# Kernel tuning notes

Measured on AMD Instinct MI355X. Metric: run time of the kernel, lower is better.

## Reference

```python
import jax, jax.numpy as jnp
import numpy as np

NUM_HEADS = 8
EPS = 1e-6


def conv1x1(x, w, b):
    # x: [b,c,h,w], w: [out,in], b: [out]  (torch Conv2d 1x1 weight squeezed)
    return jnp.einsum('bchw,oc->bohw', x, w) + b[None, :, None, None]


def feature_map(x):
    return jax.nn.elu(x) + 1.0


def setup_inputs() -> dict:
    key = jax.random.key(0)
    ks = jax.random.split(key, 9)
    C = 512
    s = 1.0 / np.sqrt(C)
    x = jax.random.normal(ks[0], (8, C, 64, 64), dtype=jnp.float32)
    wq = jax.random.normal(ks[1], (C, C), dtype=jnp.float32) * s
    wk = jax.random.normal(ks[2], (C, C), dtype=jnp.float32) * s
    wv = jax.random.normal(ks[3], (C, C), dtype=jnp.float32) * s
    wo = jax.random.normal(ks[4], (C, C), dtype=jnp.float32) * s
    bq = jax.random.normal(ks[5], (C,), dtype=jnp.float32) * 0.01
    bk = jax.random.normal(ks[6], (C,), dtype=jnp.float32) * 0.01
    bv = jax.random.normal(ks[7], (C,), dtype=jnp.float32) * 0.01
    bo = jax.random.normal(ks[8], (C,), dtype=jnp.float32) * 0.01
    return {'x': x, 'wq': wq, 'bq': bq, 'wk': wk, 'bk': bk,
            'wv': wv, 'bv': bv, 'wo': wo, 'bo': bo}


def reference(x, wq, bq, wk, bk, wv, bv, wo, bo):
    b, c, h, w = x.shape
    nh = NUM_HEADS
    hd = c // nh
    L = h * w

    def to_heads(t):
        # [b,c,h,w] -> [b,nh,L,hd]
        return t.reshape(b, nh, hd, L).transpose(0, 1, 3, 2)

    Q = feature_map(to_heads(conv1x1(x, wq, bq)))
    K = feature_map(to_heads(conv1x1(x, wk, bk)))
    V = to_heads(conv1x1(x, wv, bv)) / L  # values / v_length

    KV = jnp.einsum('bhld,bhlv->bhdv', K, V)                 # [b,nh,hd,hd]
    Z = 1.0 / (jnp.einsum('bhld,bhd->bhl', Q, K.sum(axis=-2)) + EPS)
    out = jnp.einsum('bhld,bhdv,bhl->bhlv', Q, KV, Z) * L    # [b,nh,L,hd]

    out = out.transpose(0, 1, 3, 2).reshape(b, c, h, w)
    return conv1x1(out, wo, bo)
```

## Files before the change

### kernel.cpp

```cpp
#include <hip/hip_runtime.h>
#include <hip/hip_bf16.h>
#include <stdint.h>

#define BATCH 8
#define CCH   512
#define NHD   8
#define HD    64
#define LLEN  4096
#define M1    1536

typedef __bf16 bf16x8 __attribute__((ext_vector_type(8)));
typedef __bf16 bf16x4 __attribute__((ext_vector_type(4)));
typedef float  f32x4  __attribute__((ext_vector_type(4)));

__device__ __forceinline__ f32x4 mfma16(bf16x8 a, bf16x8 b, f32x4 c) {
  return __builtin_amdgcn_mfma_f32_16x16x32_bf16(a, b, c, 0, 0, 0);
}

__device__ __forceinline__ void gload_lds16(const void* g, void* l) {
  __builtin_amdgcn_global_load_lds(
      (const __attribute__((address_space(1))) uint32_t*)(uintptr_t)g,
      (__attribute__((address_space(3))) uint32_t*)(uintptr_t)l,
      16, 0, 0);
}

__global__ void pack_w(const float* __restrict__ wq, const float* __restrict__ wk,
                       const float* __restrict__ wv, const float* __restrict__ wo,
                       const float* __restrict__ bq, const float* __restrict__ bk,
                       const float* __restrict__ bv,
                       __bf16* __restrict__ wqkvb, __bf16* __restrict__ wob,
                       float* __restrict__ biasq) {
  const int n = M1 * CCH + CCH * CCH + M1;
  for (int i = blockIdx.x * blockDim.x + threadIdx.x; i < n; i += gridDim.x * blockDim.x) {
    if (i < M1 * CCH) {
      int r = i >> 9, c = i & 511;
      float v = (r < 512) ? wq[r * 512 + c]
              : (r < 1024) ? wk[(r - 512) * 512 + c]
                           : wv[(r - 1024) * 512 + c];
      wqkvb[i] = (__bf16)v;
    } else if (i < M1 * CCH + CCH * CCH) {
      int j = i - M1 * CCH;
      wob[j] = (__bf16)wo[j];
    } else {
      int j = i - M1 * CCH - CCH * CCH;
      biasq[j] = (j < 512) ? bq[j] : (j < 1024) ? bk[j - 512] : bv[j - 1024];
    }
  }
}

__global__ __launch_bounds__(256) void transpose_x(const float* __restrict__ x,
                                                   __bf16* __restrict__ xt) {
  __shared__ float tile[64][65];
  const int b = blockIdx.z, c0 = blockIdx.y * 64, l0 = blockIdx.x * 64;
  const int t = threadIdx.x;
  const int lq = (t & 15) * 4, cr = t >> 4;
  const float* xp = x + ((size_t)b * CCH + c0) * LLEN + l0;
#pragma unroll
  for (int q = 0; q < 4; ++q) {
    const int c = cr + q * 16;
    float4 v = *(const float4*)(xp + (size_t)c * LLEN + lq);
    tile[c][lq + 0] = v.x;
    tile[c][lq + 1] = v.y;
    tile[c][lq + 2] = v.z;
    tile[c][lq + 3] = v.w;
  }
  __syncthreads();
  __bf16* xo = xt + ((size_t)b * LLEN + l0) * CCH + c0;
  const int c8 = (t & 7) * 8, lr = t >> 3;
#pragma unroll
  for (int p = 0; p < 2; ++p) {
    const int l = lr + p * 32;
    bf16x8 o;
#pragma unroll
    for (int i = 0; i < 8; ++i) o[i] = (__bf16)tile[c8 + i][l];
    *(bf16x8*)(xo + (size_t)l * CCH + c8) = o;
  }
}

#define STG128(tt, buf)                                                      \
  {                                                                          \
    const __bf16* As_ = Ag + (tt) * 32;                                      \
    const __bf16* Bs_ = Bg + (tt) * 32;                                      \
    __bf16* dA = lds + (buf) * 8192;                                         \
    __bf16* dB = dA + 4096;                                                  \
    gload_lds16(As_ + srcOff1, dA + tid * 8);                                \
    gload_lds16(As_ + srcOff2, dA + tid * 8 + 2048);                         \
    gload_lds16(Bs_ + srcOff1, dB + tid * 8);                                \
    gload_lds16(Bs_ + srcOff2, dB + tid * 8 + 2048);                         \
  }

template <int EPI>
__global__ __launch_bounds__(256, 4) void gemm128(
    const __bf16* __restrict__ A, const __bf16* __restrict__ Bm,
    const float* __restrict__ bias,
    __bf16* __restrict__ qt, __bf16* __restrict__ kcm, __bf16* __restrict__ vcm,
    float* __restrict__ out) {
  __shared__ __attribute__((aligned(16))) __bf16 lds[17408];
  const int b  = blockIdx.z;
  const int n0 = blockIdx.x * 128;
  const int m0 = blockIdx.y * 128;
  const int tid = threadIdx.x;
  const int ll = tid & 63, w = tid >> 6;
  const int wr = w >> 1, wc = w & 1;
  const int lhi = ll >> 4, llo = ll & 15;

  const int slotE = ((lhi ^ ((llo >> 1) & 3)) << 3);
  int aOff[4], bOff[4];
#pragma unroll
  for (int m = 0; m < 4; ++m) aOff[m] = (wr * 64 + m * 16 + llo) * 32 + slotE;
#pragma unroll
  for (int n = 0; n < 4; ++n) bOff[n] = 4096 + (wc * 64 + n * 16 + llo) * 32 + slotE;

  const int s1 = tid, s2 = tid + 256;
  const int r1 = s1 >> 2, r2s = s2 >> 2;
  const int srcOff1 = r1 * CCH + (((s1 & 3) ^ ((r1 >> 1) & 3)) << 3);
  const int srcOff2 = r2s * CCH + (((s2 & 3) ^ ((r2s >> 1) & 3)) << 3);

  const __bf16* Ag = A + (size_t)m0 * CCH;
  const __bf16* Bg = Bm + ((size_t)b * LLEN + n0) * CCH;

  f32x4 acc[4][4] = {};

  STG128(0, 0)
  __syncthreads();

  for (int t = 0; t < 16; ++t) {
    const int buf = t & 1;
    if (t < 15) STG128(t + 1, buf ^ 1)
    bf16x8 af[4], bfr[4];
    const __bf16* base = lds + buf * 8192;
#pragma unroll
    for (int m = 0; m < 4; ++m) af[m] = *(const bf16x8*)(base + aOff[m]);
#pragma unroll
    for (int n = 0; n < 4; ++n) bfr[n] = *(const bf16x8*)(base + bOff[n]);
#pragma unroll
    for (int m = 0; m < 4; ++m)
#pragma unroll
      for (int n = 0; n < 4; ++n) acc[m][n] = mfma16(af[m], bfr[n], acc[m][n]);
    __syncthreads();
  }

  if (EPI == 0) {
    if (m0 < 512) {
#pragma unroll
      for (int i = 0; i < 4; ++i)
#pragma unroll
        for (int j = 0; j < 4; ++j) {
          const int chq = wr * 64 + i * 16 + lhi * 4;
          const int lq  = wc * 64 + j * 16 + llo;
          bf16x4 pk;
#pragma unroll
          for (int r = 0; r < 4; ++r) {
            float tv = acc[i][j][r] + bias[m0 + chq + r];
            tv = tv > 0.f ? tv + 1.f : __expf(tv);
            pk[r] = (__bf16)tv;
          }
          *(bf16x4*)(lds + lq * 136 + chq) = pk;
        }
      __syncthreads();
      const int l = tid >> 1, seg = tid & 1;
      __bf16* dst = qt + ((size_t)b * LLEN + n0 + l) * CCH + m0 + seg * 64;
      const __bf16* src = lds + l * 136 + seg * 64;
#pragma unroll
      for (int k = 0; k < 8; ++k)
        *(bf16x8*)(dst + k * 8) = *(const bf16x8*)(src + k * 8);
    } else {
      const bool isK = (m0 < 1024);
      __bf16* base_out = isK ? kcm + ((size_t)b * CCH + (m0 - 512)) * LLEN
                             : vcm + ((size_t)b * CCH + (m0 - 1024)) * LLEN;
#pragma unroll
      for (int i = 0; i < 4; ++i)
#pragma unroll
        for (int j = 0; j < 4; ++j) {
          const int chq = wr * 64 + i * 16 + lhi * 4;
          const int lq  = wc * 64 + j * 16 + llo;
#pragma unroll
          for (int r = 0; r < 4; ++r) {
            float tv = acc[i][j][r] + bias[m0 + chq + r];
            if (isK) tv = tv > 0.f ? tv + 1.f : __expf(tv);
            lds[(chq + r) * 136 + lq] = (__bf16)tv;
          }
        }
      __syncthreads();
      const int ch = tid >> 1, seg = tid & 1;
      __bf16* dst = base_out + (size_t)ch * LLEN + n0 + seg * 64;
      const __bf16* src = lds + ch * 136 + seg * 64;
#pragma unroll
      for (int k = 0; k < 8; ++k)
        *(bf16x8*)(dst + k * 8) = *(const bf16x8*)(src + k * 8);
    }
  } else {
    float* flds = (float*)lds;
#pragma unroll
    for (int p = 0; p < 2; ++p) {
      if (p) __syncthreads();
#pragma unroll
      for (int i = 0; i < 4; ++i)
#pragma unroll
        for (int jj = 0; jj < 2; ++jj) {
          const int j = p * 2 + jj;
          const int chq = wr * 64 + i * 16 + lhi * 4;
          const int cc  = wc * 32 + jj * 16 + llo;
#pragma unroll
          for (int r = 0; r < 4; ++r)
            flds[(chq + r) * 68 + cc] = acc[i][j][r] + bias[m0 + chq + r];
        }
      __syncthreads();
      const int ch = tid >> 1, half = tid & 1;
      float* dst = out + ((size_t)b * CCH + m0 + ch) * LLEN + n0 + half * 64 + p * 32;
      const float* src = flds + ch * 68 + half * 32;
#pragma unroll
      for (int k = 0; k < 8; ++k)
        *(float4*)(dst + k * 4) = *(const float4*)(src + k * 4);
    }
  }
}

__global__ __launch_bounds__(256) void kv_part_k(const __bf16* __restrict__ kcm,
                                                 const __bf16* __restrict__ vcm,
                                                 float* __restrict__ part,
                                                 float* __restrict__ part_ks) {
  __shared__ float red[8192];
  __shared__ float ksred[4][64];
  const int lc = blockIdx.x, bh = blockIdx.y;
  const int b = bh >> 3, h = bh & 7;
  const int tid = threadIdx.x;
  const int w = tid >> 6, ll = tid & 63, lhi = ll >> 4, llo = ll & 15;
  const __bf16* Kp = kcm + ((size_t)b * CCH + h * 64) * LLEN;
  const __bf16* Vp = vcm + ((size_t)b * CCH + h * 64) * LLEN;
  f32x4 acc[4][4];
#pragma unroll
  for (int i = 0; i < 4; ++i)
#pragma unroll
    for (int j = 0; j < 4; ++j) acc[i][j] = (f32x4){0.f, 0.f, 0.f, 0.f};
  float ks[4] = {0.f, 0.f, 0.f, 0.f};
  const int base = lc * 512 + w * 128 + lhi * 8;
#pragma unroll
  for (int kt = 0; kt < 4; ++kt) {
    const int k0 = base + kt * 32;
    bf16x8 af[4], bfr[4];
#pragma unroll
    for (int i = 0; i < 4; ++i) af[i]  = *(const bf16x8*)(Kp + (size_t)(i * 16 + llo) * LLEN + k0);
#pragma unroll
    for (int i = 0; i < 4; ++i) bfr[i] = *(const bf16x8*)(Vp + (size_t)(i * 16 + llo) * LLEN + k0);
#pragma unroll
    for (int i = 0; i < 4; ++i)
#pragma unroll
      for (int r = 0; r < 8; ++r) ks[i] += (float)af[i][r];
#pragma unroll
    for (int i = 0; i < 4; ++i)
#pragma unroll
      for (int j = 0; j < 4; ++j) acc[i][j] = mfma16(af[i], bfr[j], acc[i][j]);
  }
#pragma unroll
  for (int i = 0; i < 4; ++i) {
    float s = ks[i];
    s += __shfl_xor(s, 16);
    s += __shfl_xor(s, 32);
    if (lhi == 0) ksred[w][i * 16 + llo] = s;
  }
  if (w >= 2) {
#pragma unroll
    for (int i = 0; i < 4; ++i)
#pragma unroll
      for (int j = 0; j < 4; ++j)
        *(f32x4*)(red + (((w - 2) * 16 + i * 4 + j) << 8) + ll * 4) = acc[i][j];
  }
  __syncthreads();
  if (w < 2) {
#pragma unroll
    for (int i = 0; i < 4; ++i)
#pragma unroll
      for (int j = 0; j < 4; ++j)
        acc[i][j] += *(const f32x4*)(red + ((w * 16 + i * 4 + j) << 8) + ll * 4);
  }
  float ksv = 0.f;
  if (w == 1) ksv = ksred[0][ll] + ksred[1][ll] + ksred[2][ll] + ksred[3][ll];
  __syncthreads();
  if (w == 1) {
#pragma unroll
    for (int i = 0; i < 4; ++i)
#pragma unroll
      for (int j = 0; j < 4; ++j)
        *(f32x4*)(red + ((i * 4 + j) << 8) + ll * 4) = acc[i][j];
    part_ks[((size_t)lc * 64 + bh) * 64 + ll] = ksv;
  }
  __syncthreads();
  if (w == 0) {
    float* op = part + ((size_t)lc * 64 + bh) * 4096;
#pragma unroll
    for (int i = 0; i < 4; ++i)
#pragma unroll
      for (int j = 0; j < 4; ++j) {
        acc[i][j] += *(const f32x4*)(red + ((i * 4 + j) << 8) + ll * 4);
#pragma unroll
        for (int r = 0; r < 4; ++r) {
          int d = i * 16 + lhi * 4 + r, v = j * 16 + llo;
          op[d * 64 + v] = acc[i][j][r];
        }
      }
  }
}

__global__ void kv_red_k(const float* __restrict__ part, float* __restrict__ kv) {
  const int i = blockIdx.x * blockDim.x + threadIdx.x;
  float s = 0.f;
#pragma unroll
  for (int lc = 0; lc < 8; ++lc) s += part[(size_t)lc * 262144 + i];
  kv[i] = s;
}

__global__ void ksum_red_k(const float* __restrict__ part_ks, float* __restrict__ ksum) {
  const int i = blockIdx.x * blockDim.x + threadIdx.x;
  float s = 0.f;
#pragma unroll
  for (int lc = 0; lc < 8; ++lc) s += part_ks[(size_t)lc * 4096 + i];
  ksum[i] = s;
}

__global__ __launch_bounds__(256) void apply_k(const __bf16* __restrict__ qt,
                                               const float* __restrict__ kv,
                                               const float* __restrict__ ksum,
                                               __bf16* __restrict__ attn) {
  __shared__ __attribute__((aligned(16))) __bf16 kvT[64 * 68];
  __shared__ float zb[256];
  const int lc = blockIdx.x, bh = blockIdx.y;
  const int b = bh >> 3, h = bh & 7;
  const int tid = threadIdx.x;
  const float* kvp = kv + (size_t)bh * 4096;
  for (int i = tid; i < 4096; i += 256) {
    int d = i >> 6, v = i & 63;
    kvT[v * 68 + d] = (__bf16)kvp[i];
  }
  const int l = lc * 256 + tid;
  const __bf16* qp = qt + ((size_t)b * LLEN + l) * CCH + h * 64;
  const float* ksp = ksum + bh * 64;
  float s = 0.f;
#pragma unroll
  for (int d8 = 0; d8 < 64; d8 += 8) {
    bf16x8 qv = *(const bf16x8*)(qp + d8);
#pragma unroll
    for (int i = 0; i < 8; ++i) s += (float)qv[i] * ksp[d8 + i];
  }
  zb[tid] = 1.0f / (s + 1e-6f);
  __syncthreads();

  const int ll = tid & 63, w = tid >> 6, lhi = ll >> 4, llo = ll & 15;
  f32x4 acc[4][4];
#pragma unroll
  for (int i = 0; i < 4; ++i)
#pragma unroll
    for (int j = 0; j < 4; ++j) acc[i][j] = (f32x4){0.f, 0.f, 0.f, 0.f};
  const __bf16* qbase = qt + ((size_t)b * LLEN + lc * 256 + w * 64) * CCH + h * 64;
#pragma unroll
  for (int kt = 0; kt < 2; ++kt) {
    const int k8 = kt * 32 + lhi * 8;
    bf16x8 af[4], bfr[4];
#pragma unroll
    for (int i = 0; i < 4; ++i)
      af[i] = *(const bf16x8*)(qbase + (size_t)(i * 16 + llo) * CCH + k8);
#pragma unroll
    for (int j = 0; j < 4; ++j) {
      const __bf16* pb = kvT + (j * 16 + llo) * 68 + k8;
      ((bf16x4*)&bfr[j])[0] = *(const bf16x4*)pb;
      ((bf16x4*)&bfr[j])[1] = *(const bf16x4*)(pb + 4);
    }
#pragma unroll
    for (int i = 0; i < 4; ++i)
#pragma unroll
      for (int j = 0; j < 4; ++j) acc[i][j] = mfma16(af[i], bfr[j], acc[i][j]);
  }
  __bf16* ap = attn + ((size_t)b * LLEN + lc * 256) * CCH + h * 64;
#pragma unroll
  for (int i = 0; i < 4; ++i)
#pragma unroll
    for (int j = 0; j < 4; ++j)
#pragma unroll
      for (int r = 0; r < 4; ++r) {
        int ml = w * 64 + i * 16 + lhi * 4 + r;
        int v = j * 16 + llo;
        ap[(size_t)ml * CCH + v] = (__bf16)(acc[i][j][r] * zb[ml]);
      }
}

extern "C" void kernel_launch(void* const* d_in, const int* in_sizes, int n_in,
                              void* d_out, int out_size, void* d_ws, size_t ws_size,
                              hipStream_t stream) {
  const float* x  = (const float*)d_in[0];
  const float* wq = (const float*)d_in[1];
  const float* bq = (const float*)d_in[2];
  const float* wk = (const float*)d_in[3];
  const float* bk = (const float*)d_in[4];
  const float* wv = (const float*)d_in[5];
  const float* bv = (const float*)d_in[6];
  const float* wo = (const float*)d_in[7];
  const float* bo = (const float*)d_in[8];
  float* out = (float*)d_out;

  char* p = (char*)d_ws;
  __bf16* xt    = (__bf16*)p; p += (size_t)BATCH * LLEN * CCH * 2;
  __bf16* qt    = (__bf16*)p; p += (size_t)BATCH * LLEN * CCH * 2;
  __bf16* kcm   = (__bf16*)p; p += (size_t)BATCH * CCH * LLEN * 2;
  __bf16* vcm   = (__bf16*)p; p += (size_t)BATCH * CCH * LLEN * 2;
  __bf16* wqkvb = (__bf16*)p; p += (size_t)M1 * CCH * 2;
  __bf16* wob   = (__bf16*)p; p += (size_t)CCH * CCH * 2;
  float*  biasq = (float*)p;  p += (size_t)M1 * 4;
  float*  ksum  = (float*)p;  p += (size_t)BATCH * CCH * 4;
  float*  part  = (float*)p;  p += (size_t)8 * 64 * HD * HD * 4;
  float*  kvb   = (float*)p;  p += (size_t)64 * HD * HD * 4;
  float*  pks   = (float*)p;  p += (size_t)8 * 64 * 64 * 4;
  __bf16* attn  = xt;

  pack_w<<<1024, 256, 0, stream>>>(wq, wk, wv, wo, bq, bk, bv, wqkvb, wob, biasq);
  transpose_x<<<dim3(64, 8, BATCH), 256, 0, stream>>>(x, xt);
  gemm128<0><<<dim3(32, 12, BATCH), 256, 0, stream>>>(wqkvb, xt, biasq, qt, kcm, vcm, nullptr);
  kv_part_k<<<dim3(8, 64), 256, 0, stream>>>(kcm, vcm, part, pks);
  kv_red_k<<<1024, 256, 0, stream>>>(part, kvb);
  ksum_red_k<<<16, 256, 0, stream>>>(pks, ksum);
  apply_k<<<dim3(16, 64), 256, 0, stream>>>(qt, kvb, ksum, attn);
  gemm128<1><<<dim3(32, 4, BATCH), 256, 0, stream>>>(wob, attn, bo, nullptr, nullptr,
                                                     nullptr, out);
}
```

Before: 190.7 us.

## Fuse x transpose/bf16 cast into QKV GEMM and drop LDS-staged epilogues

Removes the separate transpose_x kernel. The QKV GEMM now reads fp32 x directly through registers, converts it to bf16 and writes it into swizzled LDS with a register double buffer, which avoids writing and re-reading the xt intermediate. The epilogues of both GEMMs no longer stage tiles through LDS and store straight from the accumulators. This removes a sync and the LDS traffic, but the resulting global stores are scattered, e.g. bf16x4 strided by CCH for Q and single-element writes for K/V. Occupancy hint drops to 3 blocks per SM, and x is re-read from fp32 by each of the 12 M-tiles, raising global read volume.

```diff
diff --git a/kernel.cpp b/kernel.cpp
--- a/kernel.cpp
+++ b/kernel.cpp
@@ -48,36 +48,140 @@
   }
 }
 
-__global__ __launch_bounds__(256) void transpose_x(const float* __restrict__ x,
-                                                   __bf16* __restrict__ xt) {
-  __shared__ float tile[64][65];
-  const int b = blockIdx.z, c0 = blockIdx.y * 64, l0 = blockIdx.x * 64;
-  const int t = threadIdx.x;
-  const int lq = (t & 15) * 4, cr = t >> 4;
-  const float* xp = x + ((size_t)b * CCH + c0) * LLEN + l0;
-#pragma unroll
-  for (int q = 0; q < 4; ++q) {
-    const int c = cr + q * 16;
-    float4 v = *(const float4*)(xp + (size_t)c * LLEN + lq);
-    tile[c][lq + 0] = v.x;
-    tile[c][lq + 1] = v.y;
-    tile[c][lq + 2] = v.z;
-    tile[c][lq + 3] = v.w;
-  }
-  __syncthreads();
-  __bf16* xo = xt + ((size_t)b * LLEN + l0) * CCH + c0;
-  const int c8 = (t & 7) * 8, lr = t >> 3;
-#pragma unroll
-  for (int p = 0; p < 2; ++p) {
-    const int l = lr + p * 32;
-    bf16x8 o;
-#pragma unroll
-    for (int i = 0; i < 8; ++i) o[i] = (__bf16)tile[c8 + i][l];
-    *(bf16x8*)(xo + (size_t)l * CCH + c8) = o;
-  }
-}
-
-#define STG128(tt, buf)                                                      \
+#define STG_A(tt, buf)                                                        \
+  {                                                                           \
+    const __bf16* As_ = Ag + (tt) * 32;                                       \
+    __bf16* dA = lds + (buf) * 8192;                                          \
+    gload_lds16(As_ + srcOff1, dA + tid * 8);                                 \
+    gload_lds16(As_ + srcOff2, dA + tid * 8 + 2048);                          \
+  }
+#define LOADB(F, tt)                                                          \
+  {                                                                           \
+    const float* xr = xb + (size_t)((tt) * 32 + ch * 8) * LLEN + l0 + lp * 2; \
+    _Pragma("unroll") for (int i = 0; i < 8; ++i)                             \
+        F[i] = *(const float2*)(xr + (size_t)i * LLEN);                       \
+  }
+#define WRITEB(F, buf)                                                        \
+  {                                                                           \
+    bf16x8 v0, v1;                                                            \
+    _Pragma("unroll") for (int i = 0; i < 8; ++i) {                           \
+      v0[i] = (__bf16)F[i].x;                                                 \
+      v1[i] = (__bf16)F[i].y;                                                 \
+    }                                                                         \
+    const int s8 = (ch ^ (lp & 3)) * 8;                                       \
+    __bf16* dB = lds + (buf) * 8192 + 4096 + lp * 64 + s8;                    \
+    *(bf16x8*)dB        = v0;                                                 \
+    *(bf16x8*)(dB + 32) = v1;                                                 \
+  }
+
+__global__ __launch_bounds__(256, 3) void gemm_qkv(
+    const __bf16* __restrict__ A, const float* __restrict__ x,
+    const float* __restrict__ bias,
+    __bf16* __restrict__ qt, __bf16* __restrict__ kcm, __bf16* __restrict__ vcm) {
+  __shared__ __attribute__((aligned(16))) __bf16 lds[2 * 8192];
+  const int b  = blockIdx.z;
+  const int n0 = blockIdx.x * 128;
+  const int m0 = blockIdx.y * 128;
+  const int tid = threadIdx.x;
+  const int ll = tid & 63, w = tid >> 6;
+  const int wr = w >> 1, wc = w & 1;
+  const int lhi = ll >> 4, llo = ll & 15;
+  const int ch = tid & 3, lp = tid >> 2;
+
+  const int slotE = ((lhi ^ ((llo >> 1) & 3)) << 3);
+  int aOff[4], bOff[4];
+#pragma unroll
+  for (int m = 0; m < 4; ++m) aOff[m] = (wr * 64 + m * 16 + llo) * 32 + slotE;
+#pragma unroll
+  for (int n = 0; n < 4; ++n) bOff[n] = 4096 + (wc * 64 + n * 16 + llo) * 32 + slotE;
+
+  const int s1 = tid, s2 = tid + 256;
+  const int r1 = s1 >> 2, r2s = s2 >> 2;
+  const int srcOff1 = r1 * CCH + (((s1 & 3) ^ ((r1 >> 1) & 3)) << 3);
+  const int srcOff2 = r2s * CCH + (((s2 & 3) ^ ((r2s >> 1) & 3)) << 3);
+
+  const __bf16* Ag = A + (size_t)m0 * CCH;
+  const float* xb = x + (size_t)b * CCH * LLEN;
+  const int l0 = n0;
+
+  f32x4 acc[4][4] = {};
+  float2 F0[8], F1[8];
+
+  LOADB(F0, 0)
+  WRITEB(F0, 0)
+  LOADB(F1, 1)
+  STG_A(0, 0)
+  __syncthreads();
+
+#pragma unroll
+  for (int tt = 0; tt < 8; ++tt) {
+    {
+      const int t = 2 * tt, buf = t & 1;
+      if (t < 15) { STG_A(t + 1, buf ^ 1) WRITEB(F1, buf ^ 1) }
+      if (t < 14) LOADB(F0, t + 2)
+      bf16x8 af[4], bq[4];
+      const __bf16* base = lds + buf * 8192;
+#pragma unroll
+      for (int m = 0; m < 4; ++m) af[m] = *(const bf16x8*)(base + aOff[m]);
+#pragma unroll
+      for (int n = 0; n < 4; ++n) bq[n] = *(const bf16x8*)(base + bOff[n]);
+#pragma unroll
+      for (int m = 0; m < 4; ++m)
+#pragma unroll
+        for (int n = 0; n < 4; ++n) acc[m][n] = mfma16(af[m], bq[n], acc[m][n]);
+      __syncthreads();
+    }
+    {
+      const int t = 2 * tt + 1, buf = t & 1;
+      if (t < 15) { STG_A(t + 1, buf ^ 1) WRITEB(F0, buf ^ 1) }
+      if (t < 14) LOADB(F1, t + 2)
+      bf16x8 af[4], bq[4];
+      const __bf16* base = lds + buf * 8192;
+#pragma unroll
+      for (int m = 0; m < 4; ++m) af[m] = *(const bf16x8*)(base + aOff[m]);
+#pragma unroll
+      for (int n = 0; n < 4; ++n) bq[n] = *(const bf16x8*)(base + bOff[n]);
+#pragma unroll
+      for (int m = 0; m < 4; ++m)
+#pragma unroll
+        for (int n = 0; n < 4; ++n) acc[m][n] = mfma16(af[m], bq[n], acc[m][n]);
+      __syncthreads();
+    }
+  }
+
+#pragma unroll
+  for (int i = 0; i < 4; ++i) {
+    const int o0 = m0 + wr * 64 + i * 16 + lhi * 4;
+#pragma unroll
+    for (int j = 0; j < 4; ++j) {
+      const int col = n0 + wc * 64 + j * 16 + llo;
+      if (m0 < 512) {
+        bf16x4 pk;
+#pragma unroll
+        for (int r = 0; r < 4; ++r) {
+          float tv = acc[i][j][r] + bias[o0 + r];
+          tv = tv > 0.f ? tv + 1.f : __expf(tv);
+          pk[r] = (__bf16)tv;
+        }
+        *(bf16x4*)(qt + ((size_t)b * LLEN + col) * CCH + o0) = pk;
+      } else if (m0 < 1024) {
+#pragma unroll
+        for (int r = 0; r < 4; ++r) {
+          float tv = acc[i][j][r] + bias[o0 + r];
+          tv = tv > 0.f ? tv + 1.f : __expf(tv);
+          kcm[((size_t)b * CCH + (o0 - 512 + r)) * LLEN + col] = (__bf16)tv;
+        }
+      } else {
+#pragma unroll
+        for (int r = 0; r < 4; ++r)
+          vcm[((size_t)b * CCH + (o0 - 1024 + r)) * LLEN + col] =
+              (__bf16)(acc[i][j][r] + bias[o0 + r]);
+      }
+    }
+  }
+}
+
+#define STG2(tt, buf)                                                        \
   {                                                                          \
     const __bf16* As_ = Ag + (tt) * 32;                                      \
     const __bf16* Bs_ = Bg + (tt) * 32;                                      \
@@ -89,13 +193,10 @@
     gload_lds16(Bs_ + srcOff2, dB + tid * 8 + 2048);                         \
   }
 
-template <int EPI>
-__global__ __launch_bounds__(256, 4) void gemm128(
+__global__ __launch_bounds__(256, 4) void gemm_out(
     const __bf16* __restrict__ A, const __bf16* __restrict__ Bm,
-    const float* __restrict__ bias,
-    __bf16* __restrict__ qt, __bf16* __restrict__ kcm, __bf16* __restrict__ vcm,
-    float* __restrict__ out) {
-  __shared__ __attribute__((aligned(16))) __bf16 lds[17408];
+    const float* __restrict__ bias, float* __restrict__ out) {
+  __shared__ __attribute__((aligned(16))) __bf16 lds[2 * 8192];
   const int b  = blockIdx.z;
   const int n0 = blockIdx.x * 128;
   const int m0 = blockIdx.y * 128;
@@ -121,12 +222,12 @@
 
   f32x4 acc[4][4] = {};
 
-  STG128(0, 0)
+  STG2(0, 0)
   __syncthreads();
 
   for (int t = 0; t < 16; ++t) {
     const int buf = t & 1;
-    if (t < 15) STG128(t + 1, buf ^ 1)
+    if (t < 15) STG2(t + 1, buf ^ 1)
     bf16x8 af[4], bfr[4];
     const __bf16* base = lds + buf * 8192;
 #pragma unroll
@@ -140,78 +241,15 @@
     __syncthreads();
   }
 
-  if (EPI == 0) {
-    if (m0 < 512) {
-#pragma unroll
-      for (int i = 0; i < 4; ++i)
-#pragma unroll
-        for (int j = 0; j < 4; ++j) {
-          const int chq = wr * 64 + i * 16 + lhi * 4;
-          const int lq  = wc * 64 + j * 16 + llo;
-          bf16x4 pk;
-#pragma unroll
-          for (int r = 0; r < 4; ++r) {
-            float tv = acc[i][j][r] + bias[m0 + chq + r];
-            tv = tv > 0.f ? tv + 1.f : __expf(tv);
-            pk[r] = (__bf16)tv;
-          }
-          *(bf16x4*)(lds + lq * 136 + chq) = pk;
-        }
-      __syncthreads();
-      const int l = tid >> 1, seg = tid & 1;
-      __bf16* dst = qt + ((size_t)b * LLEN + n0 + l) * CCH + m0 + seg * 64;
-      const __bf16* src = lds + l * 136 + seg * 64;
-#pragma unroll
-      for (int k = 0; k < 8; ++k)
-        *(bf16x8*)(dst + k * 8) = *(const bf16x8*)(src + k * 8);
-    } else {
-      const bool isK = (m0 < 1024);
-      __bf16* base_out = isK ? kcm + ((size_t)b * CCH + (m0 - 512)) * LLEN
-                             : vcm + ((size_t)b * CCH + (m0 - 1024)) * LLEN;
-#pragma unroll
-      for (int i = 0; i < 4; ++i)
-#pragma unroll
-        for (int j = 0; j < 4; ++j) {
-          const int chq = wr * 64 + i * 16 + lhi * 4;
-          const int lq  = wc * 64 + j * 16 + llo;
-#pragma unroll
-          for (int r = 0; r < 4; ++r) {
-            float tv = acc[i][j][r] + bias[m0 + chq + r];
-            if (isK) tv = tv > 0.f ? tv + 1.f : __expf(tv);
-            lds[(chq + r) * 136 + lq] = (__bf16)tv;
-          }
-        }
-      __syncthreads();
-      const int ch = tid >> 1, seg = tid & 1;
-      __bf16* dst = base_out + (size_t)ch * LLEN + n0 + seg * 64;
-      const __bf16* src = lds + ch * 136 + seg * 64;
-#pragma unroll
-      for (int k = 0; k < 8; ++k)
-        *(bf16x8*)(dst + k * 8) = *(const bf16x8*)(src + k * 8);
-    }
-  } else {
-    float* flds = (float*)lds;
-#pragma unroll
-    for (int p = 0; p < 2; ++p) {
-      if (p) __syncthreads();
-#pragma unroll
-      for (int i = 0; i < 4; ++i)
-#pragma unroll
-        for (int jj = 0; jj < 2; ++jj) {
-          const int j = p * 2 + jj;
-          const int chq = wr * 64 + i * 16 + lhi * 4;
-          const int cc  = wc * 32 + jj * 16 + llo;
-#pragma unroll
-          for (int r = 0; r < 4; ++r)
-            flds[(chq + r) * 68 + cc] = acc[i][j][r] + bias[m0 + chq + r];
-        }
-      __syncthreads();
-      const int ch = tid >> 1, half = tid & 1;
-      float* dst = out + ((size_t)b * CCH + m0 + ch) * LLEN + n0 + half * 64 + p * 32;
-      const float* src = flds + ch * 68 + half * 32;
-#pragma unroll
-      for (int k = 0; k < 8; ++k)
-        *(float4*)(dst + k * 4) = *(const float4*)(src + k * 4);
+#pragma unroll
+  for (int i = 0; i < 4; ++i) {
+    const int o0 = m0 + wr * 64 + i * 16 + lhi * 4;
+#pragma unroll
+    for (int j = 0; j < 4; ++j) {
+      const int col = n0 + wc * 64 + j * 16 + llo;
+#pragma unroll
+      for (int r = 0; r < 4; ++r)
+        out[((size_t)b * CCH + o0 + r) * LLEN + col] = acc[i][j][r] + bias[o0 + r];
     }
   }
 }
@@ -398,7 +436,7 @@
   float* out = (float*)d_out;
 
   char* p = (char*)d_ws;
-  __bf16* xt    = (__bf16*)p; p += (size_t)BATCH * LLEN * CCH * 2;
+  __bf16* attn  = (__bf16*)p; p += (size_t)BATCH * LLEN * CCH * 2;
   __bf16* qt    = (__bf16*)p; p += (size_t)BATCH * LLEN * CCH * 2;
   __bf16* kcm   = (__bf16*)p; p += (size_t)BATCH * CCH * LLEN * 2;
   __bf16* vcm   = (__bf16*)p; p += (size_t)BATCH * CCH * LLEN * 2;
@@ -409,15 +447,12 @@
   float*  part  = (float*)p;  p += (size_t)8 * 64 * HD * HD * 4;
   float*  kvb   = (float*)p;  p += (size_t)64 * HD * HD * 4;
   float*  pks   = (float*)p;  p += (size_t)8 * 64 * 64 * 4;
-  __bf16* attn  = xt;
 
   pack_w<<<1024, 256, 0, stream>>>(wq, wk, wv, wo, bq, bk, bv, wqkvb, wob, biasq);
-  transpose_x<<<dim3(64, 8, BATCH), 256, 0, stream>>>(x, xt);
-  gemm128<0><<<dim3(32, 12, BATCH), 256, 0, stream>>>(wqkvb, xt, biasq, qt, kcm, vcm, nullptr);
+  gemm_qkv<<<dim3(32, 12, BATCH), 256, 0, stream>>>(wqkvb, x, biasq, qt, kcm, vcm);
   kv_part_k<<<dim3(8, 64), 256, 0, stream>>>(kcm, vcm, part, pks);
   kv_red_k<<<1024, 256, 0, stream>>>(part, kvb);
   ksum_red_k<<<16, 256, 0, stream>>>(pks, ksum);
   apply_k<<<dim3(16, 64), 256, 0, stream>>>(qt, kvb, ksum, attn);
-  gemm128<1><<<dim3(32, 4, BATCH), 256, 0, stream>>>(wob, attn, bo, nullptr, nullptr,
-                                                     nullptr, out);
-}
+  gemm_out<<<dim3(32, 4, BATCH), 256, 0, stream>>>(wob, attn, bo, out);
+}
```

Result: slower. 289.6 us (+51.9%).
